# Kernel tuning notes

Hardware: AMD Instinct MI355X
Metric: run time of the kernel (lower is better)

## Reference

```python
import jax, jax.numpy as jnp
import numpy as np

B, D, C = 4096, 4096, 1024


def setup_inputs() -> dict:
    key = jax.random.key(0)
    kx, kw = jax.random.split(key)
    x = jax.random.normal(kx, (B, D), dtype=jnp.float32)
    # kaiming_normal_ with nonlinearity='relu': std = sqrt(2 / fan_in)
    W = jax.random.normal(kw, (C, D), dtype=jnp.float32) * jnp.sqrt(2.0 / D)
    return {"x": x, "W": W}


def reference(x, W):
    # Original: -( (x[:, :, None] - W.T[None, :, :])**2 ).mean(axis=1)
    d = x.shape[1]
    x_sq = jnp.sum(x * x, axis=1, keepdims=True)        # [B, 1]
    w_sq = jnp.sum(W * W, axis=1)[None, :]              # [1, C]
    cross = jnp.einsum('bd,cd->bc', x, W)               # [B, C] tensor-core GEMM
    return -(x_sq - 2.0 * cross + w_sq) / d
```

## Files before the change

kernel.cpp:

```cpp
#include <hip/hip_runtime.h>
#include <hip/hip_bf16.h>


typedef float f32x4 __attribute__((ext_vector_type(4)));
typedef float f32x2 __attribute__((ext_vector_type(2)));
typedef float f32x16 __attribute__((ext_vector_type(16)));
typedef int i32x4 __attribute__((ext_vector_type(4)));
typedef int i32x8 __attribute__((ext_vector_type(8)));

#define BDIM 4096
#define DDIM 4096
#define CDIM 1024
#define TM 256
#define TN 256
#define BK 64
#define KSPLIT 4
#define NIT ((DDIM / KSPLIT) / BK)
#define SCALE 32.0f
#define INV_SS (1.0f/1024.0f)
#define PSCALE 0.0625f

#define WAITV(N) asm volatile("s_waitcnt vmcnt(" #N ")" ::: "memory")

__global__ __launch_bounds__(256) void cvt_rowsq(
    const float* __restrict__ x, const float* __restrict__ W,
    unsigned char* __restrict__ xb, unsigned char* __restrict__ wb,
    float* __restrict__ xsq, float* __restrict__ wsq)
{
    const int lane = threadIdx.x & 63;
    const int row = blockIdx.x * 4 + (threadIdx.x >> 6);

    const float* src;
    unsigned char* dst;
    float* sq;
    if (row < BDIM) {
        src = x + (size_t)row * DDIM;
        dst = xb + (size_t)row * DDIM;
        sq = xsq + row;
    } else {
        int r = row - BDIM;
        src = W + (size_t)r * DDIM;
        dst = wb + (size_t)r * DDIM;
        sq = wsq + r;
    }

    const float4* s4 = (const float4*)src;
    unsigned int* d4 = (unsigned int*)dst;
    float a = 0.f;
    #pragma unroll
    for (int s = 0; s < DDIM / 4 / 64; ++s) {
        float4 f = s4[lane + 64 * s];
        a += f.x * f.x + f.y * f.y + f.z * f.z + f.w * f.w;
        unsigned int p = 0;
        p = __builtin_amdgcn_cvt_pk_fp8_f32(f.x * SCALE, f.y * SCALE, p, false);
        p = __builtin_amdgcn_cvt_pk_fp8_f32(f.z * SCALE, f.w * SCALE, p, true);
        d4[lane + 64 * s] = p;
    }
    #pragma unroll
    for (int off = 32; off > 0; off >>= 1) a += __shfl_down(a, off);
    if (lane == 0) *sq = a;
}


__device__ __forceinline__ i32x8 cat8(i32x4 lo, i32x4 hi) {
    return __builtin_shufflevector(lo, hi, 0, 1, 2, 3, 4, 5, 6, 7);
}

#define MXMFMA(A, Bv, C)                                                  \
    __builtin_amdgcn_mfma_scale_f32_32x32x64_f8f6f4(                      \
        (A), (Bv), (C), 0, 0, 0, 0x7F7F7F7F, 0, 0x7F7F7F7F)

#define GLOAD16(gp, lp)                                                   \
    __builtin_amdgcn_global_load_lds(                                     \
        (const __attribute__((address_space(1))) void*)(gp),              \
        (__attribute__((address_space(3))) void*)(lp), 16, 0, 0)

__global__ __launch_bounds__(512, 2) void gemm_eucl(
    const unsigned char* __restrict__ xb,
    const unsigned char* __restrict__ wb,
    unsigned int* __restrict__ part)
{
    __shared__ unsigned char sm[3 * 32768];

    const int tid = threadIdx.x;
    const int lane = tid & 63;
    const int w = tid >> 6;
    const int wr = w >> 2;
    const int wc = w & 3;
    const int bm = blockIdx.x * TM;
    const int bn = blockIdx.y * TN;
    const int ks = blockIdx.z * (DDIM / KSPLIT);

    const int srow = w * 32 + (lane >> 2);
    const int schunk = ((lane & 3) ^ ((lane >> 3) & 3)) * 16;
    const unsigned char* gA0 = xb + (size_t)(bm + srow) * DDIM + ks + schunk;
    const unsigned char* gA1 = gA0 + (size_t)16 * DDIM;
    const unsigned char* gB0 = wb + (size_t)(bn + srow) * DDIM + ks + schunk;
    const unsigned char* gB1 = gB0 + (size_t)16 * DDIM;
    unsigned char* lA0 = sm + w * 2048;
    unsigned char* lA1 = lA0 + 1024;
    unsigned char* lB0 = sm + 16384 + w * 2048;
    unsigned char* lB1 = lB0 + 1024;

#define STAGE(q, t)                                                       \
    do {                                                                  \
        GLOAD16(gA0 + (t) * BK, lA0 + (q) * 32768);                       \
        GLOAD16(gA1 + (t) * BK, lA1 + (q) * 32768);                       \
        GLOAD16(gB0 + (t) * BK, lB0 + (q) * 32768);                       \
        GLOAD16(gB1 + (t) * BK, lB1 + (q) * 32768);                       \
    } while (0)

    const int s_rd = ((lane & 31) >> 1) & 3;
    const int c0s = ((lane >> 5) * 2) ^ s_rd;
    const unsigned char* aR0 = sm + (wr * 128 + (lane & 31)) * 64 + c0s * 16;
    const unsigned char* aR1 = sm + (wr * 128 + (lane & 31)) * 64 + (c0s ^ 1) * 16;
    const unsigned char* bR0 = sm + 16384 + (wc * 64 + (lane & 31)) * 64 + c0s * 16;
    const unsigned char* bR1 = sm + 16384 + (wc * 64 + (lane & 31)) * 64 + (c0s ^ 1) * 16;

    f32x16 acc[8] = {};

    STAGE(0, 0);
    STAGE(1, 1);

    #pragma unroll
    for (int t = 0; t < NIT; ++t) {
        const int qo = (t % 3) * 32768;
        if (t + 1 < NIT) WAITV(4);
        else             WAITV(0);
        __builtin_amdgcn_s_barrier();
        if (t + 2 < NIT) STAGE((t + 2) % 3, t + 2);
        i32x8 fb0 = cat8(*(const i32x4*)(bR0 + qo), *(const i32x4*)(bR1 + qo));
        i32x8 fb1 = cat8(*(const i32x4*)(bR0 + qo + 2048),
                         *(const i32x4*)(bR1 + qo + 2048));
        i32x8 fa0 = cat8(*(const i32x4*)(aR0 + qo), *(const i32x4*)(aR1 + qo));
        i32x8 fa1 = cat8(*(const i32x4*)(aR0 + qo + 2048),
                         *(const i32x4*)(aR1 + qo + 2048));
        i32x8 fa2 = cat8(*(const i32x4*)(aR0 + qo + 4096),
                         *(const i32x4*)(aR1 + qo + 4096));
        i32x8 fa3 = cat8(*(const i32x4*)(aR0 + qo + 6144),
                         *(const i32x4*)(aR1 + qo + 6144));
        __builtin_amdgcn_s_setprio(1);
        acc[0] = MXMFMA(fa0, fb0, acc[0]);
        acc[1] = MXMFMA(fa0, fb1, acc[1]);
        acc[2] = MXMFMA(fa1, fb0, acc[2]);
        acc[3] = MXMFMA(fa1, fb1, acc[3]);
        acc[4] = MXMFMA(fa2, fb0, acc[4]);
        acc[5] = MXMFMA(fa2, fb1, acc[5]);
        acc[6] = MXMFMA(fa3, fb0, acc[6]);
        acc[7] = MXMFMA(fa3, fb1, acc[7]);
        __builtin_amdgcn_s_setprio(0);
    }

    const int bb = blockIdx.x * 4 + blockIdx.y;
    unsigned int* p = part + ((size_t)blockIdx.z * 64 + bb) * (32 * 512);
    #pragma unroll
    for (int f = 0; f < 8; ++f)
        #pragma unroll
        for (int g = 0; g < 4; ++g) {
            unsigned int pk = 0;
            pk = __builtin_amdgcn_cvt_pk_fp8_f32(
                acc[f][g * 4 + 0] * PSCALE, acc[f][g * 4 + 1] * PSCALE, pk, false);
            pk = __builtin_amdgcn_cvt_pk_fp8_f32(
                acc[f][g * 4 + 2] * PSCALE, acc[f][g * 4 + 3] * PSCALE, pk, true);
            p[(f * 4 + g) * 512 + tid] = pk;
        }
#undef STAGE
}

__global__ __launch_bounds__(256) void reduce_out(
    const unsigned int* __restrict__ part, const float* __restrict__ xsq,
    const float* __restrict__ wsq, float* __restrict__ out)
{
    const int bid = blockIdx.x;
    const int bb = bid >> 3;
    const int w = bid & 7;
    const int wr = w >> 2, wc = w & 3;
    const int t = threadIdx.x;
    const int lane = t & 63;
    const int g = t >> 6;
    const int bm = (bb >> 2) * TM, bn = (bb & 3) * TN;
    const size_t sl = (size_t)64 * 32 * 512;
    const float c1 = 2.0f * 16.0f * INV_SS / (float)DDIM;
    const float c2 = 1.0f / (float)DDIM;

    #pragma unroll
    for (int f = 0; f < 8; ++f) {
        size_t o = ((size_t)bb * 32 + f * 4 + g) * 512 + w * 64 + lane;
        f32x2 s01 = {0.f, 0.f}, s23 = {0.f, 0.f};
        #pragma unroll
        for (int z = 0; z < KSPLIT; ++z) {
            unsigned int u = part[o + (size_t)z * sl];
            s01 += __builtin_amdgcn_cvt_pk_f32_fp8(u, false);
            s23 += __builtin_amdgcn_cvt_pk_f32_fp8(u, true);
        }
        int i = f >> 1, j = f & 1;
        int gn = bn + wc * 64 + j * 32 + (lane & 31);
        float wv = wsq[gn];
        int gm0 = bm + wr * 128 + i * 32 + 8 * g + 4 * (lane >> 5);
        float sv[4] = {s01.x, s01.y, s23.x, s23.y};
        #pragma unroll
        for (int r = 0; r < 4; ++r) {
            out[(size_t)(gm0 + r) * CDIM + gn] = sv[r] * c1 - (xsq[gm0 + r] + wv) * c2;
        }
    }
}

__global__ void fallback_kernel(const float* __restrict__ x, const float* __restrict__ W,
                                float* __restrict__ out)
{
    int c = blockIdx.x * blockDim.x + threadIdx.x;
    int b = blockIdx.y;
    if (c >= CDIM) return;
    const float* xr = x + (size_t)b * DDIM;
    const float* wr = W + (size_t)c * DDIM;
    float xs = 0.f, ws = 0.f, cr = 0.f;
    for (int d = 0; d < DDIM; ++d) {
        float xv = xr[d], wv = wr[d];
        xs += xv * xv; ws += wv * wv; cr += xv * wv;
    }
    out[(size_t)b * CDIM + c] = (2.0f * cr - xs - ws) / (float)DDIM;
}

extern "C" void kernel_launch(void* const* d_in, const int* in_sizes, int n_in,
                              void* d_out, int out_size, void* d_ws, size_t ws_size,
                              hipStream_t stream) {
    const float* x = (const float*)d_in[0];
    const float* W = (const float*)d_in[1];
    float* out = (float*)d_out;

    size_t need = (size_t)(BDIM + CDIM) * DDIM
                + (size_t)(BDIM + CDIM) * sizeof(float)
                + (size_t)KSPLIT * BDIM * CDIM;
    if (ws_size < need) {
        fallback_kernel<<<dim3(CDIM / 256, BDIM), 256, 0, stream>>>(x, W, out);
        return;
    }

    unsigned char* xb = (unsigned char*)d_ws;
    unsigned char* wb = xb + (size_t)BDIM * DDIM;
    float* xsq = (float*)(wb + (size_t)CDIM * DDIM);
    float* wsq = xsq + BDIM;
    unsigned int* part = (unsigned int*)(wsq + CDIM);

    cvt_rowsq<<<(BDIM + CDIM) / 4, 256, 0, stream>>>(x, W, xb, wb, xsq, wsq);
    gemm_eucl<<<dim3(BDIM / TM, CDIM / TN, KSPLIT), 512, 0, stream>>>(xb, wb, part);
    reduce_out<<<512, 256, 0, stream>>>(part, xsq, wsq, out);
}
```

Measured before the change: 135.6 us.

## Shrink GEMM tile to 128x128 with four waves per block

Reduces the MX-FP8 GEMM block tile from 256x256 with 8 waves to 128x128 with 4 waves, each wave still computing a 64x64 sub-tile. It also halves the triple-buffered LDS and remaps the fp8 partial layout and the reduce kernel indexing to match. The grid grows from 256 to 1024 blocks across the K-splits, which improves CU coverage and allows three blocks per CU. The cost is lower operand reuse per LDS tile, so the kernel moves more global data per MFMA.

```diff
diff --git a/kernel.cpp b/kernel.cpp
--- a/kernel.cpp
+++ b/kernel.cpp
@@ -11,8 +11,8 @@
 #define BDIM 4096
 #define DDIM 4096
 #define CDIM 1024
-#define TM 256
-#define TN 256
+#define TM 128
+#define TN 128
 #define BK 64
 #define KSPLIT 4
 #define NIT ((DDIM / KSPLIT) / BK)
@@ -75,18 +75,18 @@
         (const __attribute__((address_space(1))) void*)(gp),              \
         (__attribute__((address_space(3))) void*)(lp), 16, 0, 0)
 
-__global__ __launch_bounds__(512, 2) void gemm_eucl(
+__global__ __launch_bounds__(256, 3) void gemm_eucl(
     const unsigned char* __restrict__ xb,
     const unsigned char* __restrict__ wb,
     unsigned int* __restrict__ part)
 {
-    __shared__ unsigned char sm[3 * 32768];
+    __shared__ unsigned char sm[3 * 16384];
 
     const int tid = threadIdx.x;
     const int lane = tid & 63;
     const int w = tid >> 6;
-    const int wr = w >> 2;
-    const int wc = w & 3;
+    const int wr = w >> 1;
+    const int wc = w & 1;
     const int bm = blockIdx.x * TM;
     const int bn = blockIdx.y * TN;
     const int ks = blockIdx.z * (DDIM / KSPLIT);
@@ -99,32 +99,32 @@
     const unsigned char* gB1 = gB0 + (size_t)16 * DDIM;
     unsigned char* lA0 = sm + w * 2048;
     unsigned char* lA1 = lA0 + 1024;
-    unsigned char* lB0 = sm + 16384 + w * 2048;
+    unsigned char* lB0 = sm + 8192 + w * 2048;
     unsigned char* lB1 = lB0 + 1024;
 
 #define STAGE(q, t)                                                       \
     do {                                                                  \
-        GLOAD16(gA0 + (t) * BK, lA0 + (q) * 32768);                       \
-        GLOAD16(gA1 + (t) * BK, lA1 + (q) * 32768);                       \
-        GLOAD16(gB0 + (t) * BK, lB0 + (q) * 32768);                       \
-        GLOAD16(gB1 + (t) * BK, lB1 + (q) * 32768);                       \
+        GLOAD16(gA0 + (t) * BK, lA0 + (q) * 16384);                       \
+        GLOAD16(gA1 + (t) * BK, lA1 + (q) * 16384);                       \
+        GLOAD16(gB0 + (t) * BK, lB0 + (q) * 16384);                       \
+        GLOAD16(gB1 + (t) * BK, lB1 + (q) * 16384);                       \
     } while (0)
 
     const int s_rd = ((lane & 31) >> 1) & 3;
     const int c0s = ((lane >> 5) * 2) ^ s_rd;
-    const unsigned char* aR0 = sm + (wr * 128 + (lane & 31)) * 64 + c0s * 16;
-    const unsigned char* aR1 = sm + (wr * 128 + (lane & 31)) * 64 + (c0s ^ 1) * 16;
-    const unsigned char* bR0 = sm + 16384 + (wc * 64 + (lane & 31)) * 64 + c0s * 16;
-    const unsigned char* bR1 = sm + 16384 + (wc * 64 + (lane & 31)) * 64 + (c0s ^ 1) * 16;
-
-    f32x16 acc[8] = {};
+    const unsigned char* aR0 = sm + (wr * 64 + (lane & 31)) * 64 + c0s * 16;
+    const unsigned char* aR1 = sm + (wr * 64 + (lane & 31)) * 64 + (c0s ^ 1) * 16;
+    const unsigned char* bR0 = sm + 8192 + (wc * 64 + (lane & 31)) * 64 + c0s * 16;
+    const unsigned char* bR1 = sm + 8192 + (wc * 64 + (lane & 31)) * 64 + (c0s ^ 1) * 16;
+
+    f32x16 acc[4] = {};
 
     STAGE(0, 0);
     STAGE(1, 1);
 
     #pragma unroll
     for (int t = 0; t < NIT; ++t) {
-        const int qo = (t % 3) * 32768;
+        const int qo = (t % 3) * 16384;
         if (t + 1 < NIT) WAITV(4);
         else             WAITV(0);
         __builtin_amdgcn_s_barrier();
@@ -135,26 +135,18 @@
         i32x8 fa0 = cat8(*(const i32x4*)(aR0 + qo), *(const i32x4*)(aR1 + qo));
         i32x8 fa1 = cat8(*(const i32x4*)(aR0 + qo + 2048),
                          *(const i32x4*)(aR1 + qo + 2048));
-        i32x8 fa2 = cat8(*(const i32x4*)(aR0 + qo + 4096),
-                         *(const i32x4*)(aR1 + qo + 4096));
-        i32x8 fa3 = cat8(*(const i32x4*)(aR0 + qo + 6144),
-                         *(const i32x4*)(aR1 + qo + 6144));
         __builtin_amdgcn_s_setprio(1);
         acc[0] = MXMFMA(fa0, fb0, acc[0]);
         acc[1] = MXMFMA(fa0, fb1, acc[1]);
         acc[2] = MXMFMA(fa1, fb0, acc[2]);
         acc[3] = MXMFMA(fa1, fb1, acc[3]);
-        acc[4] = MXMFMA(fa2, fb0, acc[4]);
-        acc[5] = MXMFMA(fa2, fb1, acc[5]);
-        acc[6] = MXMFMA(fa3, fb0, acc[6]);
-        acc[7] = MXMFMA(fa3, fb1, acc[7]);
         __builtin_amdgcn_s_setprio(0);
     }
 
-    const int bb = blockIdx.x * 4 + blockIdx.y;
-    unsigned int* p = part + ((size_t)blockIdx.z * 64 + bb) * (32 * 512);
-    #pragma unroll
-    for (int f = 0; f < 8; ++f)
+    const int bb = blockIdx.x * 8 + blockIdx.y;
+    unsigned int* p = part + ((size_t)blockIdx.z * 256 + bb) * 4096;
+    #pragma unroll
+    for (int f = 0; f < 4; ++f)
         #pragma unroll
         for (int g = 0; g < 4; ++g) {
             unsigned int pk = 0;
@@ -162,7 +154,7 @@
                 acc[f][g * 4 + 0] * PSCALE, acc[f][g * 4 + 1] * PSCALE, pk, false);
             pk = __builtin_amdgcn_cvt_pk_fp8_f32(
                 acc[f][g * 4 + 2] * PSCALE, acc[f][g * 4 + 3] * PSCALE, pk, true);
-            p[(f * 4 + g) * 512 + tid] = pk;
+            p[(f * 4 + g) * 256 + tid] = pk;
         }
 #undef STAGE
 }
@@ -172,20 +164,23 @@
     const float* __restrict__ wsq, float* __restrict__ out)
 {
     const int bid = blockIdx.x;
-    const int bb = bid >> 3;
-    const int w = bid & 7;
-    const int wr = w >> 2, wc = w & 3;
+    const int bb = bid >> 1;
+    const int half = bid & 1;
     const int t = threadIdx.x;
     const int lane = t & 63;
-    const int g = t >> 6;
-    const int bm = (bb >> 2) * TM, bn = (bb & 3) * TN;
-    const size_t sl = (size_t)64 * 32 * 512;
+    const int w = t >> 6;
+    const int wr = w >> 1, wc = w & 1;
+    const int bm = (bb >> 3) * TM, bn = (bb & 7) * TN;
+    const size_t sl = (size_t)256 * 4096;
     const float c1 = 2.0f * 16.0f * INV_SS / (float)DDIM;
     const float c2 = 1.0f / (float)DDIM;
 
     #pragma unroll
-    for (int f = 0; f < 8; ++f) {
-        size_t o = ((size_t)bb * 32 + f * 4 + g) * 512 + w * 64 + lane;
+    for (int ff = 0; ff < 8; ++ff) {
+        const int fg = half * 8 + ff;
+        const int f = fg >> 2;
+        const int g = fg & 3;
+        size_t o = ((size_t)bb * 16 + fg) * 256 + t;
         f32x2 s01 = {0.f, 0.f}, s23 = {0.f, 0.f};
         #pragma unroll
         for (int z = 0; z < KSPLIT; ++z) {
@@ -193,10 +188,10 @@
             s01 += __builtin_amdgcn_cvt_pk_f32_fp8(u, false);
             s23 += __builtin_amdgcn_cvt_pk_f32_fp8(u, true);
         }
-        int i = f >> 1, j = f & 1;
-        int gn = bn + wc * 64 + j * 32 + (lane & 31);
-        float wv = wsq[gn];
-        int gm0 = bm + wr * 128 + i * 32 + 8 * g + 4 * (lane >> 5);
+        const int i = f >> 1, j = f & 1;
+        const int gn = bn + wc * 64 + j * 32 + (lane & 31);
+        const float wv = wsq[gn];
+        const int gm0 = bm + wr * 64 + i * 32 + g * 8 + (lane >> 5) * 4;
         float sv[4] = {s01.x, s01.y, s23.x, s23.y};
         #pragma unroll
         for (int r = 0; r < 4; ++r) {
@@ -243,6 +238,6 @@
     unsigned int* part = (unsigned int*)(wsq + CDIM);
 
     cvt_rowsq<<<(BDIM + CDIM) / 4, 256, 0, stream>>>(x, W, xb, wb, xsq, wsq);
-    gemm_eucl<<<dim3(BDIM / TM, CDIM / TN, KSPLIT), 512, 0, stream>>>(xb, wb, part);
+    gemm_eucl<<<dim3(BDIM / TM, CDIM / TN, KSPLIT), 256, 0, stream>>>(xb, wb, part);
     reduce_out<<<512, 256, 0, stream>>>(part, xsq, wsq, out);
 }
```

After: 139.8 us. +3.0%, slower.

## Interleave global-to-LDS prefetch loads with MFMA groups using per-phase barriers

Applied to the files above, without the earlier changes.

Splits each K-iteration into four phases, each issuing one global-to-LDS prefetch load, a barrier and LDS wait, then two MFMAs, so memory traffic is spread across the compute. It also changes the staging layout so each wave loads 16 rows in two halves 128 rows apart instead of 32 contiguous rows. The aim is to hide load latency more evenly and reduce bursty VMEM issue. In exchange it adds four extra workgroup barriers per iteration, which may stall waves and serialize the MFMA stream.

```diff
diff --git a/kernel.cpp b/kernel.cpp
--- a/kernel.cpp
+++ b/kernel.cpp
@@ -21,6 +21,8 @@
 #define PSCALE 0.0625f
 
 #define WAITV(N) asm volatile("s_waitcnt vmcnt(" #N ")" ::: "memory")
+#define LGKM0()  asm volatile("s_waitcnt lgkmcnt(0)" ::: "memory")
+#define BAR()    __builtin_amdgcn_s_barrier()
 
 __global__ __launch_bounds__(256) void cvt_rowsq(
     const float* __restrict__ x, const float* __restrict__ W,
@@ -91,18 +93,27 @@
     const int bn = blockIdx.y * TN;
     const int ks = blockIdx.z * (DDIM / KSPLIT);
 
-    const int srow = w * 32 + (lane >> 2);
+    const int srow = w * 16 + (lane >> 2);
     const int schunk = ((lane & 3) ^ ((lane >> 3) & 3)) * 16;
     const unsigned char* gA0 = xb + (size_t)(bm + srow) * DDIM + ks + schunk;
-    const unsigned char* gA1 = gA0 + (size_t)16 * DDIM;
+    const unsigned char* gA1 = gA0 + (size_t)128 * DDIM;
     const unsigned char* gB0 = wb + (size_t)(bn + srow) * DDIM + ks + schunk;
-    const unsigned char* gB1 = gB0 + (size_t)16 * DDIM;
-    unsigned char* lA0 = sm + w * 2048;
-    unsigned char* lA1 = lA0 + 1024;
-    unsigned char* lB0 = sm + 16384 + w * 2048;
-    unsigned char* lB1 = lB0 + 1024;
-
-#define STAGE(q, t)                                                       \
+    const unsigned char* gB1 = gB0 + (size_t)128 * DDIM;
+    unsigned char* lA0 = sm + w * 1024;
+    unsigned char* lA1 = lA0 + 8192;
+    unsigned char* lB0 = sm + 16384 + w * 1024;
+    unsigned char* lB1 = lB0 + 8192;
+
+    const int s_rd = ((lane & 31) >> 1) & 3;
+    const int c0s = ((lane >> 5) * 2) ^ s_rd;
+    const unsigned char* aR0 = sm + (wr * 128 + (lane & 31)) * 64 + c0s * 16;
+    const unsigned char* aR1 = sm + (wr * 128 + (lane & 31)) * 64 + (c0s ^ 1) * 16;
+    const unsigned char* bR0 = sm + 16384 + (wc * 64 + (lane & 31)) * 64 + c0s * 16;
+    const unsigned char* bR1 = sm + 16384 + (wc * 64 + (lane & 31)) * 64 + (c0s ^ 1) * 16;
+
+    f32x16 acc[8] = {};
+
+#define STAGE_FULL(q, t)                                                  \
     do {                                                                  \
         GLOAD16(gA0 + (t) * BK, lA0 + (q) * 32768);                       \
         GLOAD16(gA1 + (t) * BK, lA1 + (q) * 32768);                       \
@@ -110,45 +121,60 @@
         GLOAD16(gB1 + (t) * BK, lB1 + (q) * 32768);                       \
     } while (0)
 
-    const int s_rd = ((lane & 31) >> 1) & 3;
-    const int c0s = ((lane >> 5) * 2) ^ s_rd;
-    const unsigned char* aR0 = sm + (wr * 128 + (lane & 31)) * 64 + c0s * 16;
-    const unsigned char* aR1 = sm + (wr * 128 + (lane & 31)) * 64 + (c0s ^ 1) * 16;
-    const unsigned char* bR0 = sm + 16384 + (wc * 64 + (lane & 31)) * 64 + c0s * 16;
-    const unsigned char* bR1 = sm + 16384 + (wc * 64 + (lane & 31)) * 64 + (c0s ^ 1) * 16;
-
-    f32x16 acc[8] = {};
-
-    STAGE(0, 0);
-    STAGE(1, 1);
+    STAGE_FULL(0, 0);
+    STAGE_FULL(1, 1);
+    WAITV(4);
+    BAR();
 
     #pragma unroll
     for (int t = 0; t < NIT; ++t) {
         const int qo = (t % 3) * 32768;
-        if (t + 1 < NIT) WAITV(4);
-        else             WAITV(0);
-        __builtin_amdgcn_s_barrier();
-        if (t + 2 < NIT) STAGE((t + 2) % 3, t + 2);
+        const int q2o = ((t + 2) % 3) * 32768;
+        const bool st = (t + 2 < NIT);
+
         i32x8 fb0 = cat8(*(const i32x4*)(bR0 + qo), *(const i32x4*)(bR1 + qo));
         i32x8 fb1 = cat8(*(const i32x4*)(bR0 + qo + 2048),
                          *(const i32x4*)(bR1 + qo + 2048));
         i32x8 fa0 = cat8(*(const i32x4*)(aR0 + qo), *(const i32x4*)(aR1 + qo));
+        if (st) GLOAD16(gA0 + (t + 2) * BK, lA0 + q2o);
+        BAR(); LGKM0();
+        __builtin_amdgcn_s_setprio(1);
+        acc[0] = MXMFMA(fa0, fb0, acc[0]);
+        acc[1] = MXMFMA(fa0, fb1, acc[1]);
+        __builtin_amdgcn_s_setprio(0);
+
         i32x8 fa1 = cat8(*(const i32x4*)(aR0 + qo + 2048),
                          *(const i32x4*)(aR1 + qo + 2048));
+        if (st) GLOAD16(gA1 + (t + 2) * BK, lA1 + q2o);
+        BAR(); LGKM0();
+        __builtin_amdgcn_s_setprio(1);
+        acc[2] = MXMFMA(fa1, fb0, acc[2]);
+        acc[3] = MXMFMA(fa1, fb1, acc[3]);
+        __builtin_amdgcn_s_setprio(0);
+
         i32x8 fa2 = cat8(*(const i32x4*)(aR0 + qo + 4096),
                          *(const i32x4*)(aR1 + qo + 4096));
+        if (st) GLOAD16(gB0 + (t + 2) * BK, lB0 + q2o);
+        BAR(); LGKM0();
+        __builtin_amdgcn_s_setprio(1);
+        acc[4] = MXMFMA(fa2, fb0, acc[4]);
+        acc[5] = MXMFMA(fa2, fb1, acc[5]);
+        __builtin_amdgcn_s_setprio(0);
+
         i32x8 fa3 = cat8(*(const i32x4*)(aR0 + qo + 6144),
                          *(const i32x4*)(aR1 + qo + 6144));
-        __builtin_amdgcn_s_setprio(1);
-        acc[0] = MXMFMA(fa0, fb0, acc[0]);
-        acc[1] = MXMFMA(fa0, fb1, acc[1]);
-        acc[2] = MXMFMA(fa1, fb0, acc[2]);
-        acc[3] = MXMFMA(fa1, fb1, acc[3]);
-        acc[4] = MXMFMA(fa2, fb0, acc[4]);
-        acc[5] = MXMFMA(fa2, fb1, acc[5]);
+        if (st) GLOAD16(gB1 + (t + 2) * BK, lB1 + q2o);
+        BAR(); LGKM0();
+        __builtin_amdgcn_s_setprio(1);
         acc[6] = MXMFMA(fa3, fb0, acc[6]);
         acc[7] = MXMFMA(fa3, fb1, acc[7]);
         __builtin_amdgcn_s_setprio(0);
+
+        if (t + 1 < NIT) {
+            if (t + 2 < NIT) { WAITV(4); }
+            else             { WAITV(0); }
+            BAR();
+        }
     }
 
     const int bb = blockIdx.x * 4 + blockIdx.y;
@@ -164,7 +190,7 @@
                 acc[f][g * 4 + 2] * PSCALE, acc[f][g * 4 + 3] * PSCALE, pk, true);
             p[(f * 4 + g) * 512 + tid] = pk;
         }
-#undef STAGE
+#undef STAGE_FULL
 }
 
 __global__ __launch_bounds__(256) void reduce_out(
```

Result: no change. 134.7 us (-0.7%).
